# Kernel tuning notes

Hardware: AMD Instinct MI355X
Metric: run time of the kernel (lower is better)

Reference implementation:

```python
import jax, jax.numpy as jnp
import numpy as np

N_NODES = 50000
N_EDGES = 800000
NUM_FEATURES = 3
HIDDEN = 128
NUM_GRAPHS = 100
NUM_CLASSES = 2


def setup_inputs() -> dict:
    key = jax.random.key(0)
    ks = jax.random.split(key, 12)
    x = jax.random.normal(ks[0], (N_NODES, NUM_FEATURES), dtype=jnp.float32)
    edge_index = jax.random.randint(ks[1], (2, N_EDGES), 0, N_NODES, dtype=jnp.int64)
    batch = jnp.sort(jax.random.randint(ks[2], (N_NODES,), 0, NUM_GRAPHS, dtype=jnp.int64))
    c1, c2, c3 = 4 * HIDDEN, 2 * HIDDEN, HIDDEN  # 512, 256, 128

    def glorot(k, fan_in, fan_out):
        s = jnp.sqrt(6.0 / (fan_in + fan_out)).astype(jnp.float32)
        return jax.random.uniform(k, (fan_in, fan_out), jnp.float32, -s, s)

    W1 = glorot(ks[3], NUM_FEATURES, c1); b1 = jnp.zeros((c1,), jnp.float32)
    W2 = glorot(ks[4], c1, c2);           b2 = jnp.zeros((c2,), jnp.float32)
    W3 = glorot(ks[5], c2, c3);           b3 = jnp.zeros((c3,), jnp.float32)
    Wc = glorot(ks[6], c3, NUM_CLASSES);  bc = jnp.zeros((NUM_CLASSES,), jnp.float32)
    return {"x": x, "W1": W1, "b1": b1, "W2": W2, "b2": b2, "W3": W3, "b3": b3,
            "Wc": Wc, "bc": bc, "edge_index": edge_index, "batch": batch}


def reference(x, W1, b1, W2, b2, W3, b3, Wc, bc, edge_index, batch):
    n = x.shape[0]
    self_loop = jnp.arange(n, dtype=edge_index.dtype)
    row = jnp.concatenate([edge_index[0], self_loop])  # source nodes (messages from)
    col = jnp.concatenate([edge_index[1], self_loop])  # target nodes (aggregate into)
    # symmetric GCN normalization with self-loops: deg^{-1/2}[row] * deg^{-1/2}[col]
    deg = jax.ops.segment_sum(jnp.ones(row.shape, x.dtype), col, num_segments=n)
    dis = jnp.where(deg > 0, jax.lax.rsqrt(jnp.maximum(deg, 1.0)), 0.0)
    norm = dis[row] * dis[col]  # [E + N]

    def gcn_conv(h, W, b):
        m = h @ W                                   # project first (cheap GEMM)
        agg = jax.ops.segment_sum(norm[:, None] * m[row], col, num_segments=n)
        return agg + b

    h = jax.nn.relu(gcn_conv(x, W1, b1))
    h = jax.nn.relu(gcn_conv(h, W2, b2))
    h = jax.nn.relu(gcn_conv(h, W3, b3))

    # global mean pool over graphs
    counts = jax.ops.segment_sum(jnp.ones((n,), h.dtype), batch, num_segments=NUM_GRAPHS)
    pooled = jax.ops.segment_sum(h, batch, num_segments=NUM_GRAPHS) / jnp.maximum(counts, 1.0)[:, None]

    logits = pooled @ Wc + bc
    return jax.nn.log_softmax(logits, axis=1)
```

## Files before the change

### kernel.cpp

```cpp
#include <hip/hip_runtime.h>
#include <hip/hip_bf16.h>
#include <hip/hip_fp8.h>
#include <math.h>

#define N_NODES 50000
#define N_EDGES 800000
#define NFEAT 3
#define C1 512
#define C2 256
#define C3 128
#define NGRAPH 100
#define NCLS 2
#define PSPLIT 8
#define NRANGE 8
#define RANGE_SZ 6250

typedef short bh8 __attribute__((ext_vector_type(8)));
typedef float f32x4 __attribute__((ext_vector_type(4)));

__device__ __forceinline__ short f2bf(float x) {
    __hip_bfloat16 h = __float2bfloat16(x);
    return *reinterpret_cast<short*>(&h);
}
__device__ __forceinline__ float bflo(unsigned int u) { return __uint_as_float(u << 16); }
__device__ __forceinline__ float bfhi(unsigned int u) { return __uint_as_float(u & 0xffff0000u); }
__device__ __forceinline__ unsigned int packbf(float a, float b) {
    return (unsigned int)(unsigned short)f2bf(a) | ((unsigned int)(unsigned short)f2bf(b) << 16);
}
__device__ __forceinline__ unsigned char f2fp8(float x) {
    __hip_fp8_e4m3 q(x);
    return (unsigned char)q.__x;
}
__device__ __forceinline__ float2 fp8x2(unsigned short u) {
    __hip_fp8x2_e4m3 q; q.__x = u; return (float2)q;
}


__global__ void count_edges(const int* __restrict__ col, int* __restrict__ counts) {
    int range = blockIdx.x & (NRANGE - 1);
    int e = (blockIdx.x >> 3) * 256 + threadIdx.x;
    if (e < N_EDGES) {
        int c = col[e];
        int lo = range * RANGE_SZ;
        if (c >= lo && c < lo + RANGE_SZ) atomicAdd(&counts[c], 1);
    }
}


__global__ void scan_chunks(const int* __restrict__ counts, const float* __restrict__ x,
                            int* __restrict__ offsets, int* __restrict__ chunksums,
                            float* __restrict__ dis, float4* __restrict__ xd) {
    __shared__ int s[256];
    int b = blockIdx.x, t = threadIdx.x;
    int i = b * 256 + t;
    int v = (i < N_NODES) ? counts[i] : 0;
    if (i < N_NODES) {
        float d = rsqrtf((float)(v + 1));
        dis[i] = d;
        xd[i] = make_float4(x[i * 3 + 0], x[i * 3 + 1], x[i * 3 + 2], d);
    }
    s[t] = v;
    __syncthreads();
    for (int d = 1; d < 256; d <<= 1) {
        int add = (t >= d) ? s[t - d] : 0;
        __syncthreads();
        s[t] += add;
        __syncthreads();
    }
    if (i < N_NODES) offsets[i + 1] = s[t];
    if (t == 255) chunksums[b] = s[255];
}

__global__ void scan_sums(int* __restrict__ chunksums, int nchunks) {
    __shared__ int s[256];
    int t = threadIdx.x;
    int v = (t < nchunks) ? chunksums[t] : 0;
    s[t] = v;
    __syncthreads();
    for (int d = 1; d < 256; d <<= 1) {
        int add = (t >= d) ? s[t - d] : 0;
        __syncthreads();
        s[t] += add;
        __syncthreads();
    }
    if (t < nchunks) chunksums[t] = (t == 0) ? 0 : s[t - 1];
}

__global__ void finalize_offsets(int* __restrict__ offsets, const int* __restrict__ chunkoffs,
                                 int* __restrict__ cursor) {
    int i = blockIdx.x * blockDim.x + threadIdx.x;
    if (i < N_NODES) {
        int v = offsets[i + 1] + chunkoffs[i / 256];
        offsets[i + 1] = v;
        if (i + 1 < N_NODES) cursor[i + 1] = v;
    }
    if (i == 0) { offsets[0] = 0; cursor[0] = 0; }
}

__global__ void scatter_edges(const int* __restrict__ rowi, const int* __restrict__ coli,
                              int* __restrict__ cursor, int* __restrict__ csr_src) {
    int range = blockIdx.x & (NRANGE - 1);
    int e = (blockIdx.x >> 3) * 256 + threadIdx.x;
    if (e < N_EDGES) {
        int c = coli[e];
        int lo = range * RANGE_SZ;
        if (c >= lo && c < lo + RANGE_SZ) {
            int p = atomicAdd(&cursor[c], 1);
            csr_src[p] = rowi[e];
        }
    }
}


__global__ void prep_weights(const float* __restrict__ W2, const float* __restrict__ W3,
                             short* __restrict__ W2t, short* __restrict__ W3t) {
    int idx = blockIdx.x * 256 + threadIdx.x;
    if (idx < C1 * C2) {
        int n = idx / C1, k = idx % C1;
        W2t[idx] = f2bf(W2[k * C2 + n]);
    } else if (idx < C1 * C2 + C2 * C3) {
        int j = idx - C1 * C2;
        int n = j / C2, k = j % C2;
        W3t[j] = f2bf(W3[k * C3 + n]);
    }
}


__global__ __launch_bounds__(256) void agg_feat3(const float4* __restrict__ xd,
                                                 const int* __restrict__ offsets,
                                                 const int* __restrict__ csr_src,
                                                 float* __restrict__ aggx) {
    int t = threadIdx.x;
    int l = t & 15;
    int i = blockIdx.x * 16 + (t >> 4);
    if (i >= N_NODES) return;
    int s = offsets[i], e = offsets[i + 1];
    float a0 = 0.f, a1 = 0.f, a2 = 0.f;
    for (int p = s + l; p < e; p += 16) {
        int r = csr_src[p];
        float4 v = xd[r];
        a0 += v.w * v.x;
        a1 += v.w * v.y;
        a2 += v.w * v.z;
    }
#pragma unroll
    for (int m = 1; m < 16; m <<= 1) {
        a0 += __shfl_xor(a0, m);
        a1 += __shfl_xor(a1, m);
        a2 += __shfl_xor(a2, m);
    }
    if (l == 0) {
        float4 self = xd[i];
        float di = self.w;
        a0 += di * self.x; a1 += di * self.y; a2 += di * self.z;
        aggx[i * 3 + 0] = di * a0;
        aggx[i * 3 + 1] = di * a1;
        aggx[i * 3 + 2] = di * a2;
    }
}


__global__ __launch_bounds__(512, 4) void gemm_l1(const float* __restrict__ aggx,
                                                  const float* __restrict__ W1,
                                                  const float* __restrict__ b1,
                                                  const float* __restrict__ dis,
                                                  const short* __restrict__ Bt,
                                                  unsigned char* __restrict__ Cmat, int M) {
    __shared__ short As[128 * 32];
    __shared__ short Bs[C2 * 32];
    __shared__ float sW1[3 * C1];
    __shared__ float sb1[C1];
    __shared__ float sa[128 * 3];
    __shared__ float sd[128];
    int bm = blockIdx.x * 128;
    int t = threadIdx.x;
    int wave = t >> 6, lane = t & 63, quad = lane >> 4, l16 = lane & 15;
    int wm = (wave >> 2) * 64;
    int wn = (wave & 3) * 64;
    f32x4 acc[4][4] = {};

    for (int j = t; j < 3 * C1; j += 512) sW1[j] = W1[j];
    if (t < C1) sb1[t] = b1[t];
    if (t < 128 * 3) {
        int r = bm + t / 3; if (r > M - 1) r = M - 1;
        sa[t] = aggx[r * 3 + (t % 3)];
    }
    if (t < 128) {
        int r = bm + t; if (r > M - 1) r = M - 1;
        sd[t] = dis[r];
    }
    __syncthreads();

    int ar = t >> 2, ak = (t & 3) * 8;
    int br = t >> 1, bk = (t & 1) * 16;
    float a0 = sa[ar * 3 + 0], a1 = sa[ar * 3 + 1], a2 = sa[ar * 3 + 2];
    float drow = sd[ar];

    for (int k0 = 0; k0 < C1; k0 += 32) {
#pragma unroll
        for (int j = 0; j < 8; ++j) {
            int k = k0 + ak + j;
            float v = a0 * sW1[k] + a1 * sW1[C1 + k] + a2 * sW1[2 * C1 + k] + sb1[k];
            As[ar * 32 + ak + j] = f2bf(drow * fmaxf(v, 0.f));
        }
        const short* bptr = Bt + (size_t)br * C1 + bk + k0;
        *(bh8*)&Bs[br * 32 + bk]     = *(const bh8*)bptr;
        *(bh8*)&Bs[br * 32 + bk + 8] = *(const bh8*)(bptr + 8);
        __syncthreads();
        bh8 af[4], bf[4];
#pragma unroll
        for (int mt = 0; mt < 4; ++mt)
            af[mt] = *(const bh8*)&As[(wm + mt * 16 + l16) * 32 + quad * 8];
#pragma unroll
        for (int nt = 0; nt < 4; ++nt)
            bf[nt] = *(const bh8*)&Bs[(wn + nt * 16 + l16) * 32 + quad * 8];
#pragma unroll
        for (int mt = 0; mt < 4; ++mt)
#pragma unroll
            for (int nt = 0; nt < 4; ++nt)
                acc[mt][nt] = __builtin_amdgcn_mfma_f32_16x16x32_bf16(af[mt], bf[nt], acc[mt][nt], 0, 0, 0);
        __syncthreads();
    }

#pragma unroll
    for (int mt = 0; mt < 4; ++mt)
#pragma unroll
        for (int nt = 0; nt < 4; ++nt) {
            int colc = wn + nt * 16 + l16;
#pragma unroll
            for (int r = 0; r < 4; ++r) {
                int rowc = bm + wm + mt * 16 + quad * 4 + r;
                if (rowc < M) Cmat[(size_t)rowc * C2 + colc] = f2fp8(acc[mt][nt][r]);
            }
        }
}


template <int K, int BN>
__global__ __launch_bounds__(512, 4) void gemm_bf16(const short* __restrict__ A,
                                                    const short* __restrict__ Bt,
                                                    unsigned char* __restrict__ Cmat, int M) {
    __shared__ short As[128 * 32];
    __shared__ short Bs[BN * 32];
    constexpr int NT = BN / 64;
    int bm = blockIdx.x * 128;
    int t = threadIdx.x;
    int wave = t >> 6, lane = t & 63, quad = lane >> 4, l16 = lane & 15;
    int wm = (wave >> 2) * 64;
    int wn = (wave & 3) * (BN / 4);
    f32x4 acc[4][NT] = {};

    int ar = t >> 2, ak = (t & 3) * 8;
    int agr = bm + ar; if (agr > M - 1) agr = M - 1;
    const short* aptr = A + (size_t)agr * K + ak;

    for (int k0 = 0; k0 < K; k0 += 32) {
        *(bh8*)&As[ar * 32 + ak] = *(const bh8*)(aptr + k0);
        if constexpr (BN == 256) {
            int br = t >> 1, bk = (t & 1) * 16;
            const short* bptr = Bt + (size_t)br * K + bk + k0;
            *(bh8*)&Bs[br * 32 + bk]     = *(const bh8*)bptr;
            *(bh8*)&Bs[br * 32 + bk + 8] = *(const bh8*)(bptr + 8);
        } else {
            int br = t >> 2, bk = (t & 3) * 8;
            *(bh8*)&Bs[br * 32 + bk] = *(const bh8*)(Bt + (size_t)br * K + bk + k0);
        }
        __syncthreads();
        bh8 af[4], bf[NT];
#pragma unroll
        for (int mt = 0; mt < 4; ++mt)
            af[mt] = *(const bh8*)&As[(wm + mt * 16 + l16) * 32 + quad * 8];
#pragma unroll
        for (int nt = 0; nt < NT; ++nt)
            bf[nt] = *(const bh8*)&Bs[(wn + nt * 16 + l16) * 32 + quad * 8];
#pragma unroll
        for (int mt = 0; mt < 4; ++mt)
#pragma unroll
            for (int nt = 0; nt < NT; ++nt)
                acc[mt][nt] = __builtin_amdgcn_mfma_f32_16x16x32_bf16(af[mt], bf[nt], acc[mt][nt], 0, 0, 0);
        __syncthreads();
    }

#pragma unroll
    for (int mt = 0; mt < 4; ++mt)
#pragma unroll
        for (int nt = 0; nt < NT; ++nt) {
            int colc = wn + nt * 16 + l16;
#pragma unroll
            for (int r = 0; r < 4; ++r) {
                int rowc = bm + wm + mt * 16 + quad * 4 + r;
                if (rowc < M) Cmat[(size_t)rowc * BN + colc] = f2fp8(acc[mt][nt][r]);
            }
        }
}


template <int C, bool PRESCALE>
__global__ __launch_bounds__(256) void aggregate_w(const unsigned char* __restrict__ m,
                                                   const int* __restrict__ offsets,
                                                   const int* __restrict__ csr_src,
                                                   const float* __restrict__ dis,
                                                   const float* __restrict__ bias,
                                                   short* __restrict__ out) {
    int i = blockIdx.x * 4 + (threadIdx.x >> 6);
    if (i >= N_NODES) return;
    int lane = threadIdx.x & 63;
    int s = __builtin_amdgcn_readfirstlane(offsets[i]);
    int e = __builtin_amdgcn_readfirstlane(offsets[i + 1]);
    float di = __uint_as_float(__builtin_amdgcn_readfirstlane(__float_as_uint(dis[i])));

    if constexpr (C == 256) {
        const unsigned int* mu = (const unsigned int*)m;
        unsigned int su = mu[(size_t)i * (C / 4) + lane];
        float2 slo = fp8x2((unsigned short)(su & 0xffffu));
        float2 shi = fp8x2((unsigned short)(su >> 16));
        float a0 = slo.x, a1 = slo.y, a2 = shi.x, a3 = shi.y;
        int p = s;
        for (; p + 16 <= e; p += 16) {
            unsigned int u[16];
#pragma unroll
            for (int j = 0; j < 16; ++j) {
                int r = csr_src[p + j];
                u[j] = mu[(size_t)r * (C / 4) + lane];
            }
#pragma unroll
            for (int j = 0; j < 16; ++j) {
                float2 lo = fp8x2((unsigned short)(u[j] & 0xffffu));
                float2 hi = fp8x2((unsigned short)(u[j] >> 16));
                a0 += lo.x; a1 += lo.y; a2 += hi.x; a3 += hi.y;
            }
        }
        if (p < e) {
            unsigned int u[16];
            float sc[16];
#pragma unroll
            for (int j = 0; j < 16; ++j) {
                int q = p + j;
                sc[j] = (q < e) ? 1.f : 0.f;
                int r = csr_src[(q < e) ? q : e - 1];
                u[j] = mu[(size_t)r * (C / 4) + lane];
            }
#pragma unroll
            for (int j = 0; j < 16; ++j) {
                float2 lo = fp8x2((unsigned short)(u[j] & 0xffffu));
                float2 hi = fp8x2((unsigned short)(u[j] >> 16));
                a0 = fmaf(sc[j], lo.x, a0);
                a1 = fmaf(sc[j], lo.y, a1);
                a2 = fmaf(sc[j], hi.x, a2);
                a3 = fmaf(sc[j], hi.y, a3);
            }
        }
        float4 b = *(const float4*)&bias[4 * lane];
        a0 = fmaxf(di * a0 + b.x, 0.f);
        a1 = fmaxf(di * a1 + b.y, 0.f);
        a2 = fmaxf(di * a2 + b.z, 0.f);
        a3 = fmaxf(di * a3 + b.w, 0.f);
        if (PRESCALE) { a0 *= di; a1 *= di; a2 *= di; a3 *= di; }
        uint2 o;
        o.x = packbf(a0, a1);
        o.y = packbf(a2, a3);
        *(uint2*)(out + (size_t)i * C + 4 * lane) = o;
    } else {
        const unsigned short* mu = (const unsigned short*)m;
        float2 sf = fp8x2(mu[(size_t)i * (C / 2) + lane]);
        float a0 = sf.x, a1 = sf.y;
        int p = s;
        for (; p + 16 <= e; p += 16) {
            unsigned short u[16];
#pragma unroll
            for (int j = 0; j < 16; ++j) {
                int r = csr_src[p + j];
                u[j] = mu[(size_t)r * (C / 2) + lane];
            }
#pragma unroll
            for (int j = 0; j < 16; ++j) {
                float2 f = fp8x2(u[j]);
                a0 += f.x; a1 += f.y;
            }
        }
        if (p < e) {
            unsigned short u[16];
            float sc[16];
#pragma unroll
            for (int j = 0; j < 16; ++j) {
                int q = p + j;
                sc[j] = (q < e) ? 1.f : 0.f;
                int r = csr_src[(q < e) ? q : e - 1];
                u[j] = mu[(size_t)r * (C / 2) + lane];
            }
#pragma unroll
            for (int j = 0; j < 16; ++j) {
                float2 f = fp8x2(u[j]);
                a0 = fmaf(sc[j], f.x, a0);
                a1 = fmaf(sc[j], f.y, a1);
            }
        }
        float2 b = *(const float2*)&bias[2 * lane];
        a0 = fmaxf(di * a0 + b.x, 0.f);
        a1 = fmaxf(di * a1 + b.y, 0.f);
        if (PRESCALE) { a0 *= di; a1 *= di; }
        ((unsigned int*)out)[(size_t)i * (C / 2) + lane] = packbf(a0, a1);
    }
}


__global__ void pool_partial(const short* __restrict__ h3, const int* __restrict__ batch,
                             float* __restrict__ pooled) {
    int g = blockIdx.x, sp = blockIdx.y;
    int t = threadIdx.x;
    __shared__ int seg[2];
    if (t < 2) {
        int target = g + t;
        int lo = 0, hi = N_NODES;
        while (lo < hi) { int mid = (lo + hi) >> 1; if (batch[mid] < target) lo = mid + 1; else hi = mid; }
        seg[t] = lo;
    }
    __syncthreads();
    int start = seg[0], end = seg[1];
    int len = end - start;
    int chunk = (len + PSPLIT - 1) / PSPLIT;
    int a = start + sp * chunk;
    int b = a + chunk; if (b > end) b = end;
    if (a >= b) return;
    const unsigned int* hu = (const unsigned int*)h3;
    float s0 = 0.f, s1 = 0.f;
    int i = a;
    for (; i + 4 <= b; i += 4) {
        unsigned int u0 = hu[(size_t)(i + 0) * (C3 / 2) + t];
        unsigned int u1 = hu[(size_t)(i + 1) * (C3 / 2) + t];
        unsigned int u2 = hu[(size_t)(i + 2) * (C3 / 2) + t];
        unsigned int u3 = hu[(size_t)(i + 3) * (C3 / 2) + t];
        s0 += bflo(u0) + bflo(u1) + bflo(u2) + bflo(u3);
        s1 += bfhi(u0) + bfhi(u1) + bfhi(u2) + bfhi(u3);
    }
    for (; i < b; ++i) {
        unsigned int u = hu[(size_t)i * (C3 / 2) + t];
        s0 += bflo(u);
        s1 += bfhi(u);
    }
    atomicAdd(&pooled[g * C3 + 2 * t], s0);
    atomicAdd(&pooled[g * C3 + 2 * t + 1], s1);
}


__global__ void finalize_head(const float* __restrict__ pooled, const int* __restrict__ batch,
                              const float* __restrict__ Wc, const float* __restrict__ bc,
                              float* __restrict__ outp) {
    int g = blockIdx.x;
    int t = threadIdx.x;
    __shared__ int seg[2];
    if (t < 2) {
        int target = g + t;
        int lo = 0, hi = N_NODES;
        while (lo < hi) { int mid = (lo + hi) >> 1; if (batch[mid] < target) lo = mid + 1; else hi = mid; }
        seg[t] = lo;
    }
    __syncthreads();
    float cnt = (float)(seg[1] - seg[0]);
    float pv = pooled[(size_t)g * C3 + t] / fmaxf(cnt, 1.f);
    float p0 = pv * Wc[t * 2 + 0];
    float p1 = pv * Wc[t * 2 + 1];
#pragma unroll
    for (int o = 32; o > 0; o >>= 1) {
        p0 += __shfl_down(p0, o);
        p1 += __shfl_down(p1, o);
    }
    __shared__ float r0[2], r1[2];
    int wid = t >> 6, lane = t & 63;
    if (lane == 0) { r0[wid] = p0; r1[wid] = p1; }
    __syncthreads();
    if (t == 0) {
        float l0 = r0[0] + r0[1] + bc[0];
        float l1 = r1[0] + r1[1] + bc[1];
        float mx = fmaxf(l0, l1);
        float lse = mx + logf(expf(l0 - mx) + expf(l1 - mx));
        outp[g * 2 + 0] = l0 - lse;
        outp[g * 2 + 1] = l1 - lse;
    }
}


extern "C" void kernel_launch(void* const* d_in, const int* in_sizes, int n_in,
                              void* d_out, int out_size, void* d_ws, size_t ws_size,
                              hipStream_t stream) {
    const float* x = (const float*)d_in[0];
    const float* W1 = (const float*)d_in[1];
    const float* b1 = (const float*)d_in[2];
    const float* W2 = (const float*)d_in[3];
    const float* b2 = (const float*)d_in[4];
    const float* W3 = (const float*)d_in[5];
    const float* b3 = (const float*)d_in[6];
    const float* Wc = (const float*)d_in[7];
    const float* bc = (const float*)d_in[8];
    const int* ei = (const int*)d_in[9];
    const int* batch = (const int*)d_in[10];
    const int* row = ei;
    const int* col = ei + N_EDGES;
    float* out = (float*)d_out;

    char* ws = (char*)d_ws;
    size_t off = 0;
    auto alloc = [&](size_t bytes) -> void* {
        off = (off + 255) & ~(size_t)255;
        void* p = ws + off;
        off += bytes;
        return p;
    };

    int* counts = (int*)alloc((size_t)N_NODES * 4);
    int* offsets = (int*)alloc((size_t)(N_NODES + 1) * 4);
    int* cursor = (int*)alloc((size_t)N_NODES * 4);
    int* chunksums = (int*)alloc(256 * 4);
    float* dis = (float*)alloc((size_t)N_NODES * 4);
    float4* xd = (float4*)alloc((size_t)N_NODES * 16);
    int* csr_src = (int*)alloc((size_t)N_EDGES * 4);
    float* aggx = (float*)alloc((size_t)N_NODES * 3 * 4);
    short* W2t = (short*)alloc((size_t)C1 * C2 * 2);
    short* W3t = (short*)alloc((size_t)C2 * C3 * 2);
    unsigned char* m2 = (unsigned char*)alloc((size_t)N_NODES * C2);
    short* h2 = (short*)alloc((size_t)N_NODES * C2 * 2);
    unsigned char* m3 = (unsigned char*)alloc((size_t)N_NODES * C3);
    short* h3 = (short*)alloc((size_t)N_NODES * C3 * 2);
    float* pooled = (float*)alloc((size_t)NGRAPH * C3 * 4);

    hipMemsetAsync(counts, 0, (size_t)N_NODES * 4, stream);
    hipMemsetAsync(pooled, 0, (size_t)NGRAPH * C3 * 4, stream);
    int nechunks = (N_EDGES + 255) / 256;
    count_edges<<<nechunks * NRANGE, 256, 0, stream>>>(col, counts);
    int nchunks = (N_NODES + 255) / 256;
    scan_chunks<<<nchunks, 256, 0, stream>>>(counts, x, offsets, chunksums, dis, xd);
    scan_sums<<<1, 256, 0, stream>>>(chunksums, nchunks);
    finalize_offsets<<<(N_NODES + 255) / 256, 256, 0, stream>>>(offsets, chunksums, cursor);
    scatter_edges<<<nechunks * NRANGE, 256, 0, stream>>>(row, col, cursor, csr_src);

    prep_weights<<<(C1 * C2 + C2 * C3 + 255) / 256, 256, 0, stream>>>(W2, W3, W2t, W3t);

    agg_feat3<<<(N_NODES + 15) / 16, 256, 0, stream>>>(xd, offsets, csr_src, aggx);

    gemm_l1<<<(N_NODES + 127) / 128, 512, 0, stream>>>(aggx, W1, b1, dis, W2t, m2, N_NODES);
    aggregate_w<C2, true><<<(N_NODES + 3) / 4, 256, 0, stream>>>(m2, offsets, csr_src, dis, b2, h2);

    gemm_bf16<C2, C3><<<(N_NODES + 127) / 128, 512, 0, stream>>>(h2, W3t, m3, N_NODES);
    aggregate_w<C3, false><<<(N_NODES + 3) / 4, 256, 0, stream>>>(m3, offsets, csr_src, dis, b3, h3);

    dim3 gp(NGRAPH, PSPLIT);
    pool_partial<<<gp, C3 / 2, 0, stream>>>(h3, batch, pooled);
    finalize_head<<<NGRAPH, C3, 0, stream>>>(pooled, batch, Wc, bc, out);
}
```

Baseline: 282.9 us.

## Fuse all GCN stages into one persistent kernel with grid-wide barriers

Replaces the chain of roughly a dozen kernel launches (CSR build, scans, weight prep, feature aggregation, GEMMs, aggregations, pooling, head) with one persistent kernel of 512 blocks. The stages are separated by a software grid barrier built on an atomic counter, and the two memsets become a single one. This removes per-launch overhead and the gaps between launches. In exchange, every stage now runs on a fixed grid of 512-thread blocks, which may lower occupancy or parallelism for the heavy phases. The barrier also requires all blocks to be co-resident, otherwise the kernel can deadlock.

```diff
diff --git a/kernel.cpp b/kernel.cpp
--- a/kernel.cpp
+++ b/kernel.cpp
@@ -14,6 +14,8 @@
 #define PSPLIT 8
 #define NRANGE 8
 #define RANGE_SZ 6250
+#define GRID 512
+#define BT 512
 
 typedef short bh8 __attribute__((ext_vector_type(8)));
 typedef float f32x4 __attribute__((ext_vector_type(4)));
@@ -35,276 +37,31 @@
     __hip_fp8x2_e4m3 q; q.__x = u; return (float2)q;
 }
 
-
-__global__ void count_edges(const int* __restrict__ col, int* __restrict__ counts) {
-    int range = blockIdx.x & (NRANGE - 1);
-    int e = (blockIdx.x >> 3) * 256 + threadIdx.x;
-    if (e < N_EDGES) {
-        int c = col[e];
-        int lo = range * RANGE_SZ;
-        if (c >= lo && c < lo + RANGE_SZ) atomicAdd(&counts[c], 1);
-    }
-}
-
-
-__global__ void scan_chunks(const int* __restrict__ counts, const float* __restrict__ x,
-                            int* __restrict__ offsets, int* __restrict__ chunksums,
-                            float* __restrict__ dis, float4* __restrict__ xd) {
-    __shared__ int s[256];
-    int b = blockIdx.x, t = threadIdx.x;
-    int i = b * 256 + t;
-    int v = (i < N_NODES) ? counts[i] : 0;
-    if (i < N_NODES) {
-        float d = rsqrtf((float)(v + 1));
-        dis[i] = d;
-        xd[i] = make_float4(x[i * 3 + 0], x[i * 3 + 1], x[i * 3 + 2], d);
-    }
-    s[t] = v;
+__device__ __forceinline__ void gsync(int* bar, int target) {
     __syncthreads();
-    for (int d = 1; d < 256; d <<= 1) {
-        int add = (t >= d) ? s[t - d] : 0;
-        __syncthreads();
-        s[t] += add;
-        __syncthreads();
-    }
-    if (i < N_NODES) offsets[i + 1] = s[t];
-    if (t == 255) chunksums[b] = s[255];
-}
-
-__global__ void scan_sums(int* __restrict__ chunksums, int nchunks) {
-    __shared__ int s[256];
-    int t = threadIdx.x;
-    int v = (t < nchunks) ? chunksums[t] : 0;
-    s[t] = v;
+    if (threadIdx.x == 0) {
+        __threadfence();
+        __hip_atomic_fetch_add(bar, 1, __ATOMIC_RELAXED, __HIP_MEMORY_SCOPE_AGENT);
+        while (__hip_atomic_load(bar, __ATOMIC_RELAXED, __HIP_MEMORY_SCOPE_AGENT) < target)
+            __builtin_amdgcn_s_sleep(2);
+        __threadfence();
+    }
     __syncthreads();
-    for (int d = 1; d < 256; d <<= 1) {
-        int add = (t >= d) ? s[t - d] : 0;
-        __syncthreads();
-        s[t] += add;
-        __syncthreads();
-    }
-    if (t < nchunks) chunksums[t] = (t == 0) ? 0 : s[t - 1];
-}
-
-__global__ void finalize_offsets(int* __restrict__ offsets, const int* __restrict__ chunkoffs,
-                                 int* __restrict__ cursor) {
-    int i = blockIdx.x * blockDim.x + threadIdx.x;
-    if (i < N_NODES) {
-        int v = offsets[i + 1] + chunkoffs[i / 256];
-        offsets[i + 1] = v;
-        if (i + 1 < N_NODES) cursor[i + 1] = v;
-    }
-    if (i == 0) { offsets[0] = 0; cursor[0] = 0; }
-}
-
-__global__ void scatter_edges(const int* __restrict__ rowi, const int* __restrict__ coli,
-                              int* __restrict__ cursor, int* __restrict__ csr_src) {
-    int range = blockIdx.x & (NRANGE - 1);
-    int e = (blockIdx.x >> 3) * 256 + threadIdx.x;
-    if (e < N_EDGES) {
-        int c = coli[e];
-        int lo = range * RANGE_SZ;
-        if (c >= lo && c < lo + RANGE_SZ) {
-            int p = atomicAdd(&cursor[c], 1);
-            csr_src[p] = rowi[e];
-        }
-    }
-}
-
-
-__global__ void prep_weights(const float* __restrict__ W2, const float* __restrict__ W3,
-                             short* __restrict__ W2t, short* __restrict__ W3t) {
-    int idx = blockIdx.x * 256 + threadIdx.x;
-    if (idx < C1 * C2) {
-        int n = idx / C1, k = idx % C1;
-        W2t[idx] = f2bf(W2[k * C2 + n]);
-    } else if (idx < C1 * C2 + C2 * C3) {
-        int j = idx - C1 * C2;
-        int n = j / C2, k = j % C2;
-        W3t[j] = f2bf(W3[k * C3 + n]);
-    }
-}
-
-
-__global__ __launch_bounds__(256) void agg_feat3(const float4* __restrict__ xd,
-                                                 const int* __restrict__ offsets,
-                                                 const int* __restrict__ csr_src,
-                                                 float* __restrict__ aggx) {
-    int t = threadIdx.x;
-    int l = t & 15;
-    int i = blockIdx.x * 16 + (t >> 4);
-    if (i >= N_NODES) return;
-    int s = offsets[i], e = offsets[i + 1];
-    float a0 = 0.f, a1 = 0.f, a2 = 0.f;
-    for (int p = s + l; p < e; p += 16) {
-        int r = csr_src[p];
-        float4 v = xd[r];
-        a0 += v.w * v.x;
-        a1 += v.w * v.y;
-        a2 += v.w * v.z;
-    }
-#pragma unroll
-    for (int m = 1; m < 16; m <<= 1) {
-        a0 += __shfl_xor(a0, m);
-        a1 += __shfl_xor(a1, m);
-        a2 += __shfl_xor(a2, m);
-    }
-    if (l == 0) {
-        float4 self = xd[i];
-        float di = self.w;
-        a0 += di * self.x; a1 += di * self.y; a2 += di * self.z;
-        aggx[i * 3 + 0] = di * a0;
-        aggx[i * 3 + 1] = di * a1;
-        aggx[i * 3 + 2] = di * a2;
-    }
-}
-
-
-__global__ __launch_bounds__(512, 4) void gemm_l1(const float* __restrict__ aggx,
-                                                  const float* __restrict__ W1,
-                                                  const float* __restrict__ b1,
-                                                  const float* __restrict__ dis,
-                                                  const short* __restrict__ Bt,
-                                                  unsigned char* __restrict__ Cmat, int M) {
-    __shared__ short As[128 * 32];
-    __shared__ short Bs[C2 * 32];
-    __shared__ float sW1[3 * C1];
-    __shared__ float sb1[C1];
-    __shared__ float sa[128 * 3];
-    __shared__ float sd[128];
-    int bm = blockIdx.x * 128;
-    int t = threadIdx.x;
-    int wave = t >> 6, lane = t & 63, quad = lane >> 4, l16 = lane & 15;
-    int wm = (wave >> 2) * 64;
-    int wn = (wave & 3) * 64;
-    f32x4 acc[4][4] = {};
-
-    for (int j = t; j < 3 * C1; j += 512) sW1[j] = W1[j];
-    if (t < C1) sb1[t] = b1[t];
-    if (t < 128 * 3) {
-        int r = bm + t / 3; if (r > M - 1) r = M - 1;
-        sa[t] = aggx[r * 3 + (t % 3)];
-    }
-    if (t < 128) {
-        int r = bm + t; if (r > M - 1) r = M - 1;
-        sd[t] = dis[r];
-    }
-    __syncthreads();
-
-    int ar = t >> 2, ak = (t & 3) * 8;
-    int br = t >> 1, bk = (t & 1) * 16;
-    float a0 = sa[ar * 3 + 0], a1 = sa[ar * 3 + 1], a2 = sa[ar * 3 + 2];
-    float drow = sd[ar];
-
-    for (int k0 = 0; k0 < C1; k0 += 32) {
-#pragma unroll
-        for (int j = 0; j < 8; ++j) {
-            int k = k0 + ak + j;
-            float v = a0 * sW1[k] + a1 * sW1[C1 + k] + a2 * sW1[2 * C1 + k] + sb1[k];
-            As[ar * 32 + ak + j] = f2bf(drow * fmaxf(v, 0.f));
-        }
-        const short* bptr = Bt + (size_t)br * C1 + bk + k0;
-        *(bh8*)&Bs[br * 32 + bk]     = *(const bh8*)bptr;
-        *(bh8*)&Bs[br * 32 + bk + 8] = *(const bh8*)(bptr + 8);
-        __syncthreads();
-        bh8 af[4], bf[4];
-#pragma unroll
-        for (int mt = 0; mt < 4; ++mt)
-            af[mt] = *(const bh8*)&As[(wm + mt * 16 + l16) * 32 + quad * 8];
-#pragma unroll
-        for (int nt = 0; nt < 4; ++nt)
-            bf[nt] = *(const bh8*)&Bs[(wn + nt * 16 + l16) * 32 + quad * 8];
-#pragma unroll
-        for (int mt = 0; mt < 4; ++mt)
-#pragma unroll
-            for (int nt = 0; nt < 4; ++nt)
-                acc[mt][nt] = __builtin_amdgcn_mfma_f32_16x16x32_bf16(af[mt], bf[nt], acc[mt][nt], 0, 0, 0);
-        __syncthreads();
-    }
-
-#pragma unroll
-    for (int mt = 0; mt < 4; ++mt)
-#pragma unroll
-        for (int nt = 0; nt < 4; ++nt) {
-            int colc = wn + nt * 16 + l16;
-#pragma unroll
-            for (int r = 0; r < 4; ++r) {
-                int rowc = bm + wm + mt * 16 + quad * 4 + r;
-                if (rowc < M) Cmat[(size_t)rowc * C2 + colc] = f2fp8(acc[mt][nt][r]);
-            }
-        }
-}
-
-
-template <int K, int BN>
-__global__ __launch_bounds__(512, 4) void gemm_bf16(const short* __restrict__ A,
-                                                    const short* __restrict__ Bt,
-                                                    unsigned char* __restrict__ Cmat, int M) {
-    __shared__ short As[128 * 32];
-    __shared__ short Bs[BN * 32];
-    constexpr int NT = BN / 64;
-    int bm = blockIdx.x * 128;
-    int t = threadIdx.x;
-    int wave = t >> 6, lane = t & 63, quad = lane >> 4, l16 = lane & 15;
-    int wm = (wave >> 2) * 64;
-    int wn = (wave & 3) * (BN / 4);
-    f32x4 acc[4][NT] = {};
-
-    int ar = t >> 2, ak = (t & 3) * 8;
-    int agr = bm + ar; if (agr > M - 1) agr = M - 1;
-    const short* aptr = A + (size_t)agr * K + ak;
-
-    for (int k0 = 0; k0 < K; k0 += 32) {
-        *(bh8*)&As[ar * 32 + ak] = *(const bh8*)(aptr + k0);
-        if constexpr (BN == 256) {
-            int br = t >> 1, bk = (t & 1) * 16;
-            const short* bptr = Bt + (size_t)br * K + bk + k0;
-            *(bh8*)&Bs[br * 32 + bk]     = *(const bh8*)bptr;
-            *(bh8*)&Bs[br * 32 + bk + 8] = *(const bh8*)(bptr + 8);
-        } else {
-            int br = t >> 2, bk = (t & 3) * 8;
-            *(bh8*)&Bs[br * 32 + bk] = *(const bh8*)(Bt + (size_t)br * K + bk + k0);
-        }
-        __syncthreads();
-        bh8 af[4], bf[NT];
-#pragma unroll
-        for (int mt = 0; mt < 4; ++mt)
-            af[mt] = *(const bh8*)&As[(wm + mt * 16 + l16) * 32 + quad * 8];
-#pragma unroll
-        for (int nt = 0; nt < NT; ++nt)
-            bf[nt] = *(const bh8*)&Bs[(wn + nt * 16 + l16) * 32 + quad * 8];
-#pragma unroll
-        for (int mt = 0; mt < 4; ++mt)
-#pragma unroll
-            for (int nt = 0; nt < NT; ++nt)
-                acc[mt][nt] = __builtin_amdgcn_mfma_f32_16x16x32_bf16(af[mt], bf[nt], acc[mt][nt], 0, 0, 0);
-        __syncthreads();
-    }
-
-#pragma unroll
-    for (int mt = 0; mt < 4; ++mt)
-#pragma unroll
-        for (int nt = 0; nt < NT; ++nt) {
-            int colc = wn + nt * 16 + l16;
-#pragma unroll
-            for (int r = 0; r < 4; ++r) {
-                int rowc = bm + wm + mt * 16 + quad * 4 + r;
-                if (rowc < M) Cmat[(size_t)rowc * BN + colc] = f2fp8(acc[mt][nt][r]);
-            }
-        }
-}
-
+}
+
+__device__ __forceinline__ int bseg(const int* __restrict__ batch, int target) {
+    int lo = 0, hi = N_NODES;
+    while (lo < hi) { int mid = (lo + hi) >> 1; if (batch[mid] < target) lo = mid + 1; else hi = mid; }
+    return lo;
+}
 
 template <int C, bool PRESCALE>
-__global__ __launch_bounds__(256) void aggregate_w(const unsigned char* __restrict__ m,
-                                                   const int* __restrict__ offsets,
-                                                   const int* __restrict__ csr_src,
-                                                   const float* __restrict__ dis,
-                                                   const float* __restrict__ bias,
-                                                   short* __restrict__ out) {
-    int i = blockIdx.x * 4 + (threadIdx.x >> 6);
-    if (i >= N_NODES) return;
-    int lane = threadIdx.x & 63;
+__device__ __forceinline__ void agg_node(int i, int lane, const unsigned char* __restrict__ m,
+                                         const int* __restrict__ offsets,
+                                         const int* __restrict__ csr_src,
+                                         const float* __restrict__ dis,
+                                         const float* __restrict__ bias,
+                                         short* __restrict__ out) {
     int s = __builtin_amdgcn_readfirstlane(offsets[i]);
     int e = __builtin_amdgcn_readfirstlane(offsets[i + 1]);
     float di = __uint_as_float(__builtin_amdgcn_readfirstlane(__float_as_uint(dis[i])));
@@ -404,78 +161,342 @@
 }
 
 
-__global__ void pool_partial(const short* __restrict__ h3, const int* __restrict__ batch,
-                             float* __restrict__ pooled) {
-    int g = blockIdx.x, sp = blockIdx.y;
+__global__ __launch_bounds__(BT, 4) void mega(
+    const float* __restrict__ x, const float* __restrict__ W1, const float* __restrict__ b1,
+    const float* __restrict__ W2, const float* __restrict__ b2,
+    const float* __restrict__ W3, const float* __restrict__ b3,
+    const float* __restrict__ Wc, const float* __restrict__ bc,
+    const int* __restrict__ row, const int* __restrict__ col, const int* __restrict__ batch,
+    int* __restrict__ counts, int* __restrict__ offsets, int* __restrict__ cursor,
+    int* __restrict__ chunksums, float* __restrict__ dis, float4* __restrict__ xd,
+    int* __restrict__ csr_src, float* __restrict__ aggx,
+    short* __restrict__ W2t, short* __restrict__ W3t,
+    unsigned char* __restrict__ m2, short* __restrict__ h2,
+    unsigned char* __restrict__ m3, short* __restrict__ h3,
+    float* __restrict__ pooled, float* __restrict__ outp, int* bar) {
+    __shared__ __attribute__((aligned(16))) char smem[34816];
     int t = threadIdx.x;
-    __shared__ int seg[2];
-    if (t < 2) {
-        int target = g + t;
-        int lo = 0, hi = N_NODES;
-        while (lo < hi) { int mid = (lo + hi) >> 1; if (batch[mid] < target) lo = mid + 1; else hi = mid; }
-        seg[t] = lo;
-    }
-    __syncthreads();
-    int start = seg[0], end = seg[1];
-    int len = end - start;
-    int chunk = (len + PSPLIT - 1) / PSPLIT;
-    int a = start + sp * chunk;
-    int b = a + chunk; if (b > end) b = end;
-    if (a >= b) return;
-    const unsigned int* hu = (const unsigned int*)h3;
-    float s0 = 0.f, s1 = 0.f;
-    int i = a;
-    for (; i + 4 <= b; i += 4) {
-        unsigned int u0 = hu[(size_t)(i + 0) * (C3 / 2) + t];
-        unsigned int u1 = hu[(size_t)(i + 1) * (C3 / 2) + t];
-        unsigned int u2 = hu[(size_t)(i + 2) * (C3 / 2) + t];
-        unsigned int u3 = hu[(size_t)(i + 3) * (C3 / 2) + t];
-        s0 += bflo(u0) + bflo(u1) + bflo(u2) + bflo(u3);
-        s1 += bfhi(u0) + bfhi(u1) + bfhi(u2) + bfhi(u3);
-    }
-    for (; i < b; ++i) {
-        unsigned int u = hu[(size_t)i * (C3 / 2) + t];
-        s0 += bflo(u);
-        s1 += bfhi(u);
-    }
-    atomicAdd(&pooled[g * C3 + 2 * t], s0);
-    atomicAdd(&pooled[g * C3 + 2 * t + 1], s1);
-}
-
-
-__global__ void finalize_head(const float* __restrict__ pooled, const int* __restrict__ batch,
-                              const float* __restrict__ Wc, const float* __restrict__ bc,
-                              float* __restrict__ outp) {
-    int g = blockIdx.x;
-    int t = threadIdx.x;
-    __shared__ int seg[2];
-    if (t < 2) {
-        int target = g + t;
-        int lo = 0, hi = N_NODES;
-        while (lo < hi) { int mid = (lo + hi) >> 1; if (batch[mid] < target) lo = mid + 1; else hi = mid; }
-        seg[t] = lo;
-    }
-    __syncthreads();
-    float cnt = (float)(seg[1] - seg[0]);
-    float pv = pooled[(size_t)g * C3 + t] / fmaxf(cnt, 1.f);
-    float p0 = pv * Wc[t * 2 + 0];
-    float p1 = pv * Wc[t * 2 + 1];
-#pragma unroll
-    for (int o = 32; o > 0; o >>= 1) {
-        p0 += __shfl_down(p0, o);
-        p1 += __shfl_down(p1, o);
-    }
-    __shared__ float r0[2], r1[2];
-    int wid = t >> 6, lane = t & 63;
-    if (lane == 0) { r0[wid] = p0; r1[wid] = p1; }
-    __syncthreads();
-    if (t == 0) {
-        float l0 = r0[0] + r0[1] + bc[0];
-        float l1 = r1[0] + r1[1] + bc[1];
-        float mx = fmaxf(l0, l1);
-        float lse = mx + logf(expf(l0 - mx) + expf(l1 - mx));
-        outp[g * 2 + 0] = l0 - lse;
-        outp[g * 2 + 1] = l1 - lse;
+    int tgt = GRID;
+
+    {
+        int nech = (N_EDGES + BT - 1) / BT;
+        for (int vb = blockIdx.x; vb < nech * NRANGE; vb += GRID) {
+            int range = vb & (NRANGE - 1);
+            int e = (vb >> 3) * BT + t;
+            if (e < N_EDGES) {
+                int c = col[e];
+                int lo = range * RANGE_SZ;
+                if (c >= lo && c < lo + RANGE_SZ) atomicAdd(&counts[c], 1);
+            }
+        }
+    }
+    gsync(bar, tgt); tgt += GRID;
+
+    {
+        int* s = (int*)smem;
+        int nck = (N_NODES + BT - 1) / BT;
+        for (int vb = blockIdx.x; vb < nck; vb += GRID) {
+            int i = vb * BT + t;
+            int v = (i < N_NODES) ? counts[i] : 0;
+            if (i < N_NODES) {
+                float d = rsqrtf((float)(v + 1));
+                dis[i] = d;
+                xd[i] = make_float4(x[i * 3 + 0], x[i * 3 + 1], x[i * 3 + 2], d);
+            }
+            s[t] = v;
+            __syncthreads();
+            for (int d2 = 1; d2 < BT; d2 <<= 1) {
+                int add = (t >= d2) ? s[t - d2] : 0;
+                __syncthreads();
+                s[t] += add;
+                __syncthreads();
+            }
+            if (i < N_NODES) offsets[i + 1] = s[t];
+            if (t == BT - 1) chunksums[vb] = s[t];
+            __syncthreads();
+        }
+    }
+    gsync(bar, tgt); tgt += GRID;
+
+    {
+        int* s = (int*)smem;
+        int nck = (N_NODES + BT - 1) / BT;
+        int v = (t < nck) ? chunksums[t] : 0;
+        s[t] = v;
+        __syncthreads();
+        for (int d2 = 1; d2 < BT; d2 <<= 1) {
+            int add = (t >= d2) ? s[t - d2] : 0;
+            __syncthreads();
+            s[t] += add;
+            __syncthreads();
+        }
+        for (int i = blockIdx.x * BT + t; i < N_NODES; i += GRID * BT) {
+            int c = i >> 9;
+            int add = (c == 0) ? 0 : s[c - 1];
+            int val = offsets[i + 1] + add;
+            offsets[i + 1] = val;
+            if (i + 1 < N_NODES) cursor[i + 1] = val;
+            if (i == 0) { offsets[0] = 0; cursor[0] = 0; }
+        }
+        for (int idx = blockIdx.x * BT + t; idx < C1 * C2 + C2 * C3; idx += GRID * BT) {
+            if (idx < C1 * C2) {
+                int n = idx / C1, k = idx % C1;
+                W2t[idx] = f2bf(W2[k * C2 + n]);
+            } else {
+                int j = idx - C1 * C2;
+                int n = j / C2, k = j % C2;
+                W3t[j] = f2bf(W3[k * C3 + n]);
+            }
+        }
+    }
+    gsync(bar, tgt); tgt += GRID;
+
+    {
+        int nech = (N_EDGES + BT - 1) / BT;
+        for (int vb = blockIdx.x; vb < nech * NRANGE; vb += GRID) {
+            int range = vb & (NRANGE - 1);
+            int e = (vb >> 3) * BT + t;
+            if (e < N_EDGES) {
+                int c = col[e];
+                int lo = range * RANGE_SZ;
+                if (c >= lo && c < lo + RANGE_SZ) {
+                    int p = atomicAdd(&cursor[c], 1);
+                    csr_src[p] = row[e];
+                }
+            }
+        }
+    }
+    gsync(bar, tgt); tgt += GRID;
+
+    {
+        int l = t & 15;
+        int ng = (N_NODES + 31) / 32;
+        for (int vb = blockIdx.x; vb < ng; vb += GRID) {
+            int i = vb * 32 + (t >> 4);
+            if (i < N_NODES) {
+                int s0 = offsets[i], e0 = offsets[i + 1];
+                float a0 = 0.f, a1 = 0.f, a2 = 0.f;
+                for (int p = s0 + l; p < e0; p += 16) {
+                    int r = csr_src[p];
+                    float4 v = xd[r];
+                    a0 += v.w * v.x;
+                    a1 += v.w * v.y;
+                    a2 += v.w * v.z;
+                }
+#pragma unroll
+                for (int m = 1; m < 16; m <<= 1) {
+                    a0 += __shfl_xor(a0, m);
+                    a1 += __shfl_xor(a1, m);
+                    a2 += __shfl_xor(a2, m);
+                }
+                if (l == 0) {
+                    float4 self = xd[i];
+                    float di = self.w;
+                    a0 += di * self.x; a1 += di * self.y; a2 += di * self.z;
+                    aggx[i * 3 + 0] = di * a0;
+                    aggx[i * 3 + 1] = di * a1;
+                    aggx[i * 3 + 2] = di * a2;
+                }
+            }
+        }
+    }
+    gsync(bar, tgt); tgt += GRID;
+
+    {
+        short* As = (short*)smem;
+        short* Bs = (short*)(smem + 8192);
+        float* sW1 = (float*)(smem + 24576);
+        float* sb1 = (float*)(smem + 30720);
+        float* sa = (float*)(smem + 32768);
+        float* sd = (float*)(smem + 34304);
+        int ntile = (N_NODES + 127) / 128;
+        int wave = t >> 6, lane = t & 63, quad = lane >> 4, l16 = lane & 15;
+        int wm = (wave >> 2) * 64, wn = (wave & 3) * 64;
+        for (int tile = blockIdx.x; tile < ntile; tile += GRID) {
+            int bm = tile * 128;
+            f32x4 acc[4][4] = {};
+            for (int j = t; j < 3 * C1; j += BT) sW1[j] = W1[j];
+            if (t < C1) sb1[t] = b1[t];
+            if (t < 128 * 3) {
+                int r = bm + t / 3; if (r > N_NODES - 1) r = N_NODES - 1;
+                sa[t] = aggx[r * 3 + (t % 3)];
+            }
+            if (t < 128) {
+                int r = bm + t; if (r > N_NODES - 1) r = N_NODES - 1;
+                sd[t] = dis[r];
+            }
+            __syncthreads();
+            int ar = t >> 2, ak = (t & 3) * 8;
+            int br = t >> 1, bk = (t & 1) * 16;
+            float a0 = sa[ar * 3 + 0], a1 = sa[ar * 3 + 1], a2 = sa[ar * 3 + 2];
+            float drow = sd[ar];
+            for (int k0 = 0; k0 < C1; k0 += 32) {
+#pragma unroll
+                for (int j = 0; j < 8; ++j) {
+                    int k = k0 + ak + j;
+                    float v = a0 * sW1[k] + a1 * sW1[C1 + k] + a2 * sW1[2 * C1 + k] + sb1[k];
+                    As[ar * 32 + ak + j] = f2bf(drow * fmaxf(v, 0.f));
+                }
+                const short* bptr = W2t + (size_t)br * C1 + bk + k0;
+                *(bh8*)&Bs[br * 32 + bk]     = *(const bh8*)bptr;
+                *(bh8*)&Bs[br * 32 + bk + 8] = *(const bh8*)(bptr + 8);
+                __syncthreads();
+                bh8 af[4], bf[4];
+#pragma unroll
+                for (int mt = 0; mt < 4; ++mt)
+                    af[mt] = *(const bh8*)&As[(wm + mt * 16 + l16) * 32 + quad * 8];
+#pragma unroll
+                for (int nt = 0; nt < 4; ++nt)
+                    bf[nt] = *(const bh8*)&Bs[(wn + nt * 16 + l16) * 32 + quad * 8];
+#pragma unroll
+                for (int mt = 0; mt < 4; ++mt)
+#pragma unroll
+                    for (int nt = 0; nt < 4; ++nt)
+                        acc[mt][nt] = __builtin_amdgcn_mfma_f32_16x16x32_bf16(af[mt], bf[nt], acc[mt][nt], 0, 0, 0);
+                __syncthreads();
+            }
+#pragma unroll
+            for (int mt = 0; mt < 4; ++mt)
+#pragma unroll
+                for (int nt = 0; nt < 4; ++nt) {
+                    int colc = wn + nt * 16 + l16;
+#pragma unroll
+                    for (int r = 0; r < 4; ++r) {
+                        int rowc = bm + wm + mt * 16 + quad * 4 + r;
+                        if (rowc < N_NODES) m2[(size_t)rowc * C2 + colc] = f2fp8(acc[mt][nt][r]);
+                    }
+                }
+            __syncthreads();
+        }
+    }
+    gsync(bar, tgt); tgt += GRID;
+
+    {
+        int lane = t & 63;
+        int ngv = (N_NODES + 7) / 8;
+        for (int vb = blockIdx.x; vb < ngv; vb += GRID) {
+            int i = vb * 8 + (t >> 6);
+            if (i < N_NODES)
+                agg_node<C2, true>(i, lane, m2, offsets, csr_src, dis, b2, h2);
+        }
+    }
+    gsync(bar, tgt); tgt += GRID;
+
+    {
+        short* As = (short*)smem;
+        short* Bs = (short*)(smem + 8192);
+        int ntile = (N_NODES + 127) / 128;
+        int wave = t >> 6, lane = t & 63, quad = lane >> 4, l16 = lane & 15;
+        int wm = (wave >> 2) * 64, wn = (wave & 3) * 32;
+        for (int tile = blockIdx.x; tile < ntile; tile += GRID) {
+            int bm = tile * 128;
+            f32x4 acc[4][2] = {};
+            int ar = t >> 2, ak = (t & 3) * 8;
+            int agr = bm + ar; if (agr > N_NODES - 1) agr = N_NODES - 1;
+            const short* aptr = h2 + (size_t)agr * C2 + ak;
+            int br2 = t >> 2, bk2 = (t & 3) * 8;
+            for (int k0 = 0; k0 < C2; k0 += 32) {
+                *(bh8*)&As[ar * 32 + ak] = *(const bh8*)(aptr + k0);
+                *(bh8*)&Bs[br2 * 32 + bk2] = *(const bh8*)(W3t + (size_t)br2 * C2 + bk2 + k0);
+                __syncthreads();
+                bh8 af[4], bf[2];
+#pragma unroll
+                for (int mt = 0; mt < 4; ++mt)
+                    af[mt] = *(const bh8*)&As[(wm + mt * 16 + l16) * 32 + quad * 8];
+#pragma unroll
+                for (int nt = 0; nt < 2; ++nt)
+                    bf[nt] = *(const bh8*)&Bs[(wn + nt * 16 + l16) * 32 + quad * 8];
+#pragma unroll
+                for (int mt = 0; mt < 4; ++mt)
+#pragma unroll
+                    for (int nt = 0; nt < 2; ++nt)
+                        acc[mt][nt] = __builtin_amdgcn_mfma_f32_16x16x32_bf16(af[mt], bf[nt], acc[mt][nt], 0, 0, 0);
+                __syncthreads();
+            }
+#pragma unroll
+            for (int mt = 0; mt < 4; ++mt)
+#pragma unroll
+                for (int nt = 0; nt < 2; ++nt) {
+                    int colc = wn + nt * 16 + l16;
+#pragma unroll
+                    for (int r = 0; r < 4; ++r) {
+                        int rowc = bm + wm + mt * 16 + quad * 4 + r;
+                        if (rowc < N_NODES) m3[(size_t)rowc * C3 + colc] = f2fp8(acc[mt][nt][r]);
+                    }
+                }
+            __syncthreads();
+        }
+    }
+    gsync(bar, tgt); tgt += GRID;
+
+    {
+        int lane = t & 63;
+        int ngv = (N_NODES + 7) / 8;
+        for (int vb = blockIdx.x; vb < ngv; vb += GRID) {
+            int i = vb * 8 + (t >> 6);
+            if (i < N_NODES)
+                agg_node<C3, false>(i, lane, m3, offsets, csr_src, dis, b3, h3);
+        }
+    }
+    gsync(bar, tgt); tgt += GRID;
+
+    {
+        int lane = t & 63;
+        int nu = NGRAPH * PSPLIT;
+        for (int u = blockIdx.x * 8 + (t >> 6); u < nu; u += GRID * 8) {
+            int g = u >> 3, sp = u & 7;
+            int start = bseg(batch, g), end = bseg(batch, g + 1);
+            int len = end - start;
+            int chunk = (len + PSPLIT - 1) / PSPLIT;
+            int a = start + sp * chunk;
+            int b = a + chunk; if (b > end) b = end;
+            if (a < b) {
+                const unsigned int* hu = (const unsigned int*)h3;
+                float s0 = 0.f, s1 = 0.f;
+                int i = a;
+                for (; i + 4 <= b; i += 4) {
+                    unsigned int u0 = hu[(size_t)(i + 0) * (C3 / 2) + lane];
+                    unsigned int u1 = hu[(size_t)(i + 1) * (C3 / 2) + lane];
+                    unsigned int u2 = hu[(size_t)(i + 2) * (C3 / 2) + lane];
+                    unsigned int u3 = hu[(size_t)(i + 3) * (C3 / 2) + lane];
+                    s0 += bflo(u0) + bflo(u1) + bflo(u2) + bflo(u3);
+                    s1 += bfhi(u0) + bfhi(u1) + bfhi(u2) + bfhi(u3);
+                }
+                for (; i < b; ++i) {
+                    unsigned int u0 = hu[(size_t)i * (C3 / 2) + lane];
+                    s0 += bflo(u0);
+                    s1 += bfhi(u0);
+                }
+                atomicAdd(&pooled[g * C3 + 2 * lane], s0);
+                atomicAdd(&pooled[g * C3 + 2 * lane + 1], s1);
+            }
+        }
+    }
+    gsync(bar, tgt); tgt += GRID;
+
+    {
+        int lane = t & 63;
+        for (int g = blockIdx.x * 8 + (t >> 6); g < NGRAPH; g += GRID * 8) {
+            int s0 = bseg(batch, g), s1 = bseg(batch, g + 1);
+            float cnt = fmaxf((float)(s1 - s0), 1.f);
+            float pv0 = pooled[(size_t)g * C3 + lane] / cnt;
+            float pv1 = pooled[(size_t)g * C3 + 64 + lane] / cnt;
+            float p0 = pv0 * Wc[lane * 2 + 0] + pv1 * Wc[(lane + 64) * 2 + 0];
+            float p1 = pv0 * Wc[lane * 2 + 1] + pv1 * Wc[(lane + 64) * 2 + 1];
+#pragma unroll
+            for (int o = 32; o > 0; o >>= 1) {
+                p0 += __shfl_down(p0, o);
+                p1 += __shfl_down(p1, o);
+            }
+            if (lane == 0) {
+                float l0 = p0 + bc[0];
+                float l1 = p1 + bc[1];
+                float mx = fmaxf(l0, l1);
+                float lse = mx + logf(expf(l0 - mx) + expf(l1 - mx));
+                outp[g * 2 + 0] = l0 - lse;
+                outp[g * 2 + 1] = l1 - lse;
+            }
+        }
     }
 }
 
@@ -508,6 +529,10 @@
     };
 
     int* counts = (int*)alloc((size_t)N_NODES * 4);
+    float* pooled = (float*)alloc((size_t)NGRAPH * C3 * 4);
+    int* bar = (int*)alloc(256);
+    size_t zero_bytes = off;
+
     int* offsets = (int*)alloc((size_t)(N_NODES + 1) * 4);
     int* cursor = (int*)alloc((size_t)N_NODES * 4);
     int* chunksums = (int*)alloc(256 * 4);
@@ -521,29 +546,11 @@
     short* h2 = (short*)alloc((size_t)N_NODES * C2 * 2);
     unsigned char* m3 = (unsigned char*)alloc((size_t)N_NODES * C3);
     short* h3 = (short*)alloc((size_t)N_NODES * C3 * 2);
-    float* pooled = (float*)alloc((size_t)NGRAPH * C3 * 4);
-
-    hipMemsetAsync(counts, 0, (size_t)N_NODES * 4, stream);
-    hipMemsetAsync(pooled, 0, (size_t)NGRAPH * C3 * 4, stream);
-    int nechunks = (N_EDGES + 255) / 256;
-    count_edges<<<nechunks * NRANGE, 256, 0, stream>>>(col, counts);
-    int nchunks = (N_NODES + 255) / 256;
-    scan_chunks<<<nchunks, 256, 0, stream>>>(counts, x, offsets, chunksums, dis, xd);
-    scan_sums<<<1, 256, 0, stream>>>(chunksums, nchunks);
-    finalize_offsets<<<(N_NODES + 255) / 256, 256, 0, stream>>>(offsets, chunksums, cursor);
-    scatter_edges<<<nechunks * NRANGE, 256, 0, stream>>>(row, col, cursor, csr_src);
-
-    prep_weights<<<(C1 * C2 + C2 * C3 + 255) / 256, 256, 0, stream>>>(W2, W3, W2t, W3t);
-
-    agg_feat3<<<(N_NODES + 15) / 16, 256, 0, stream>>>(xd, offsets, csr_src, aggx);
-
-    gemm_l1<<<(N_NODES + 127) / 128, 512, 0, stream>>>(aggx, W1, b1, dis, W2t, m2, N_NODES);
-    aggregate_w<C2, true><<<(N_NODES + 3) / 4, 256, 0, stream>>>(m2, offsets, csr_src, dis, b2, h2);
-
-    gemm_bf16<C2, C3><<<(N_NODES + 127) / 128, 512, 0, stream>>>(h2, W3t, m3, N_NODES);
-    aggregate_w<C3, false><<<(N_NODES + 3) / 4, 256, 0, stream>>>(m3, offsets, csr_src, dis, b3, h3);
-
-    dim3 gp(NGRAPH, PSPLIT);
-    pool_partial<<<gp, C3 / 2, 0, stream>>>(h3, batch, pooled);
-    finalize_head<<<NGRAPH, C3, 0, stream>>>(pooled, batch, Wc, bc, out);
-}
+
+    hipMemsetAsync(ws, 0, zero_bytes, stream);
+    mega<<<GRID, BT, 0, stream>>>(x, W1, b1, W2, b2, W3, b3, Wc, bc,
+                                  row, col, batch,
+                                  counts, offsets, cursor, chunksums, dis, xd,
+                                  csr_src, aggx, W2t, W3t, m2, h2, m3, h3,
+                                  pooled, out, bar);
+}
```

Result: slower. 846.3 us (+199.2%).
